# Kernel optimization log

Hardware: AMD Instinct MI355X
Metric: run time of the kernel (lower is better)

## Reference

```python
import jax, jax.numpy as jnp
import numpy as np

T, N, E, F_IN, H1, H2, NUM_GRAPHS, K = 8, 10000, 320000, 32, 32, 16, 64, 5


def setup_inputs() -> dict:
    key = jax.random.key(0)
    ks = jax.random.split(key, 16)
    p = lambda k, shape: jax.random.normal(k, shape, jnp.float32) * 0.05
    return {
        "x": jax.random.normal(ks[0], (T, N, F_IN), jnp.float32),
        "edge_index": jax.random.randint(ks[1], (2, E), 0, N),
        "edge_attr": jax.random.uniform(ks[2], (E,), jnp.float32),
        "batch": jnp.sort(jax.random.randint(ks[3], (N,), 0, NUM_GRAPHS)),
        "Wx1": p(ks[4], (4, K, F_IN, H1)),
        "bx1": jnp.zeros((4, H1), jnp.float32),
        "Wh1": p(ks[5], (4, K, H1, H1)),
        "bh1": jnp.zeros((4, H1), jnp.float32),
        "wc1": p(ks[6], (3, H1)),
        "b1": jnp.zeros((4, H1), jnp.float32),
        "Wx2": p(ks[7], (4, K, H1, H2)),
        "bx2": jnp.zeros((4, H2), jnp.float32),
        "Wh2": p(ks[8], (4, K, H2, H2)),
        "bh2": jnp.zeros((4, H2), jnp.float32),
        "wc2": p(ks[9], (3, H2)),
        "b2": jnp.zeros((4, H2), jnp.float32),
        "lin_w": p(ks[10], (H2, 1)),
        "lin_b": jnp.zeros((1,), jnp.float32),
    }


def _forward(x, edge_index, edge_attr, batch,
             Wx1, bx1, Wh1, bh1, wc1, b1,
             Wx2, bx2, Wh2, bh2, wc2, b2, lin_w, lin_b):
    src, dst = edge_index[0], edge_index[1]
    n = x.shape[1]

    # ChebConv sym normalization with lambda_max=2: L_hat = L_sym - I = -D^{-1/2} A D^{-1/2}
    deg = jax.ops.segment_sum(edge_attr, src, num_segments=n)
    deg_safe = jnp.where(deg > 0, deg, 1.0)
    dis = jnp.where(deg > 0, jax.lax.rsqrt(deg_safe), 0.0)
    wnorm = dis[src] * edge_attr * dis[dst]  # [E]

    def Lhat(z):  # z: [N, C] -> L_hat @ z
        return -jax.ops.segment_sum(wnorm[:, None] * z[src], dst, num_segments=n)

    def cheb(z, W, b):  # W: [K, C_in, C_out], b: [C_out]
        out = z @ W[0]
        Tp, Tc = z, Lhat(z)  # T_0, T_1
        out = out + Tc @ W[1]
        for k in range(2, W.shape[0]):
            Tp, Tc = Tc, 2.0 * Lhat(Tc) - Tp
            out = out + Tc @ W[k]
        return out + b

    def cell(X, H, C, Wx, bx, Wh, bh, wc, bg):
        # gate order: 0=i, 1=f, 2=c, 3=o (GConvLSTM with peepholes)
        I = jax.nn.sigmoid(cheb(X, Wx[0], bx[0]) + cheb(H, Wh[0], bh[0]) + wc[0] * C + bg[0])
        Fg = jax.nn.sigmoid(cheb(X, Wx[1], bx[1]) + cheb(H, Wh[1], bh[1]) + wc[1] * C + bg[1])
        Ct = jnp.tanh(cheb(X, Wx[2], bx[2]) + cheb(H, Wh[2], bh[2]) + bg[2])
        Cn = Fg * C + I * Ct
        O = jax.nn.sigmoid(cheb(X, Wx[3], bx[3]) + cheb(H, Wh[3], bh[3]) + wc[2] * Cn + bg[3])
        return O * jnp.tanh(Cn), Cn

    @jax.checkpoint
    def step(carry, xt):
        h1, c1, h2, c2 = carry
        h1, c1 = cell(xt, h1, c1, Wx1, bx1, Wh1, bh1, wc1, b1)
        h2, c2 = cell(h1, h2, c2, Wx2, bx2, Wh2, bh2, wc2, b2)
        return (h1, c1, h2, c2), None

    z32 = jnp.zeros((n, Wh1.shape[-1]), x.dtype)
    z16 = jnp.zeros((n, Wh2.shape[-1]), x.dtype)
    (h1, c1, h2, c2), _ = jax.lax.scan(step, (z32, z32, z16, z16), x)

    # relu/dropout on h2 in the torch code is dead code (its result is unused in eval)
    u = jax.ops.segment_sum(h2, batch, num_segments=NUM_GRAPHS)  # global_add_pool
    return (u @ lin_w + lin_b).reshape(-1)


def reference(x, edge_index, edge_attr, batch,
              Wx1, bx1, Wh1, bh1, wc1, b1,
              Wx2, bx2, Wh2, bh2, wc2, b2, lin_w, lin_b):
    return _forward(x, edge_index, edge_attr, batch,
                    Wx1, bx1, Wh1, bh1, wc1, b1,
                    Wx2, bx2, Wh2, bh2, wc2, b2, lin_w, lin_b)
```

## Files before the change

kernel.cpp:

```cpp
#include <hip/hip_runtime.h>
#include <hip/hip_bf16.h>

#define TT 8
#define NN 10000
#define EE 320000
#define NG 64
#define SZS 400
#define SZH 384

typedef short v8s __attribute__((ext_vector_type(8)));
typedef _Float16 v8h __attribute__((ext_vector_type(8)));
typedef float v4f __attribute__((ext_vector_type(4)));

__device__ __forceinline__ float sigmf(float x){ return 1.f/(1.f+expf(-x)); }
__device__ __forceinline__ unsigned short f2h(float f){ _Float16 h=(_Float16)f; return __builtin_bit_cast(unsigned short,h); }
__device__ __forceinline__ float h2f(unsigned short s){ return (float)__builtin_bit_cast(_Float16,s); }
__device__ __forceinline__ unsigned pack2h(float x,float y){ return (unsigned)f2h(x) | ((unsigned)f2h(y)<<16); }
__device__ __forceinline__ size_t fragidx(int TK,int row,int c){
  int tile=row>>4, m=row&15, kt=c>>5, cc=c&31;
  return ((size_t)(tile*TK+kt)*64 + (cc>>3)*16 + m)*8 + (cc&7);
}

__global__ void k_deg(const int* __restrict__ src, const float* __restrict__ ea, float* __restrict__ deg){
  int e = blockIdx.x*256 + threadIdx.x;
  if(e<EE) atomicAdd(&deg[src[e]], ea[e]);
}

__global__ void k_dis(const float* __restrict__ deg, float* __restrict__ dis){
  int n = blockIdx.x*256+threadIdx.x;
  if(n<NN){ float d=deg[n]; dis[n] = d>0.f ? rsqrtf(d) : 0.f; }
}

__global__ void k_wnorm(const int* __restrict__ src, const int* __restrict__ dst, const float* __restrict__ ea,
                        const float* __restrict__ dis, float* __restrict__ wnorm, int* __restrict__ cnt){
  int e = blockIdx.x*256+threadIdx.x;
  if(e<EE){
    int s=src[e], d=dst[e];
    wnorm[e] = dis[s]*ea[e]*dis[d];
    atomicAdd(&cnt[d],1);
  }
}

__global__ __launch_bounds__(1024) void k_scan(const int* __restrict__ cnt, int* __restrict__ rowptr, int* __restrict__ wp){
  __shared__ int wsum[16];
  __shared__ int carrysh;
  int tid=threadIdx.x, lane=tid&63, wv=tid>>6;
  if(tid==0){ carrysh=0; rowptr[0]=0; }
  __syncthreads();
  for(int base=0;base<NN;base+=1024){
    int i=base+tid;
    int v=(i<NN)?cnt[i]:0;
    int s=v;
    #pragma unroll
    for(int d=1;d<64;d<<=1){ int t=__shfl_up(s,d,64); if(lane>=d) s+=t; }
    if(lane==63) wsum[wv]=s;
    __syncthreads();
    if(wv==0 && lane<16){
      int t=wsum[lane]; int ss=t;
      #pragma unroll
      for(int d=1;d<16;d<<=1){ int u=__shfl_up(ss,d,64); if(lane>=d) ss+=u; }
      wsum[lane]=ss-t;
    }
    __syncthreads();
    int total = carrysh + wsum[wv] + s;
    if(i<NN) rowptr[i+1]=total;
    __syncthreads();
    if(tid==1023) carrysh = total;
    __syncthreads();
  }
  for(int i=tid;i<NN;i+=1024) wp[i]=rowptr[i];
}

__global__ void k_scatter(const int* __restrict__ src, const int* __restrict__ dst, const float* __restrict__ wnorm,
                          int* __restrict__ wp, int2* __restrict__ pack){
  int e = blockIdx.x*256+threadIdx.x;
  if(e<EE){
    int d=dst[e];
    int pos = atomicAdd(&wp[d],1);
    pack[pos] = make_int2(src[e], __float_as_int(wnorm[e]));
  }
}

__device__ __forceinline__ float fetchW1(const float* Wx, const float* Wh, int kk, int col){
  int g=col>>5, j=col&31;
  if(kk<160){ int k=kk>>5, i=kk&31; return Wx[((g*5+k)*32+i)*32+j]; }
  int rr=kk-160; int k=rr>>5, i=rr&31; return Wh[((g*5+k)*32+i)*32+j];
}
__device__ __forceinline__ float fetchW2(const float* Wx, const float* Wh, int kk, int col){
  int g=col>>4, j=col&15;
  if(kk<160){ int k=kk>>5, i=kk&31; return Wx[((g*5+k)*32+i)*16+j]; }
  if(kk<240){ int rr=kk-160; int k=rr>>4, i=rr&15; return Wh[((g*5+k)*16+i)*16+j]; }
  return 0.f;
}

__global__ void k_wreorg(const float* __restrict__ Wx1,const float* __restrict__ bx1,
                         const float* __restrict__ Wh1,const float* __restrict__ bh1,const float* __restrict__ b1,
                         const float* __restrict__ Wx2,const float* __restrict__ bx2,
                         const float* __restrict__ Wh2,const float* __restrict__ bh2,const float* __restrict__ b2g,
                         short* __restrict__ Wpk1, short* __restrict__ Wpk2,
                         float* __restrict__ Bc1,float* __restrict__ Bc2){
  int idx = blockIdx.x*256+threadIdx.x;
  if(idx < 5120){
    int lane=idx&63, rest=idx>>6;
    int nt=rest&7, kt=rest>>3;
    int col = nt*16 + (lane&15);
    int g = lane>>4;
    #pragma unroll
    for(int j=0;j<8;j++){
      int kk = kt*32 + 8*g + j;
      Wpk1[(size_t)idx*8+j]=(short)f2h(fetchW1(Wx1,Wh1,kk,col));
    }
  } else if(idx < 7168){
    int t=idx-5120;
    int lane=t&63, rest=t>>6;
    int nt=rest&3, kt=rest>>2;
    int col = nt*16 + (lane&15);
    int g = lane>>4;
    #pragma unroll
    for(int j=0;j<8;j++){
      int kk = kt*32 + 8*g + j;
      Wpk2[(size_t)t*8+j]=(short)f2h(fetchW2(Wx2,Wh2,kk,col));
    }
  } else if(idx < 7296){
    int i=idx-7168; int g=i>>5,j=i&31;
    Bc1[i]=bx1[g*32+j]+bh1[g*32+j]+b1[g*32+j];
  } else if(idx < 7360){
    int i=idx-7296; int g=i>>4,j=i&15;
    Bc2[i]=bx2[g*16+j]+bh2[g*16+j]+b2g[g*16+j];
  }
}

__global__ void k_init1(const float* __restrict__ xt, float* __restrict__ ZS,
                        unsigned short* __restrict__ ZH, short* __restrict__ Zb1){
  int idx=blockIdx.x*256+threadIdx.x;
  if(idx<NN*8){
    int n=idx>>3, c4=idx&7;
    float4 v = ((const float4*)xt)[idx];
    *(float4*)&ZS[(size_t)n*SZS + 240 + c4*4] = v;
    unsigned p0=pack2h(v.x,v.y), p1=pack2h(v.z,v.w);
    *(unsigned*)&ZH[(size_t)n*SZH + 48 + c4*4]     = p0;
    *(unsigned*)&ZH[(size_t)n*SZH + 48 + c4*4 + 2] = p1;
    size_t fi = fragidx(5, n, c4*4);
    *(unsigned*)&Zb1[fi]   = p0;
    *(unsigned*)&Zb1[fi+2] = p1;
  }
}

template<int MODE>
__global__ __launch_bounds__(256) void k_spmm(const int* __restrict__ rowptr, const int2* __restrict__ pack,
    float* __restrict__ ZS, unsigned short* __restrict__ ZH,
    short* __restrict__ Zb1, short* __restrict__ Zb2, int k){
  int wlocal = __builtin_amdgcn_readfirstlane(threadIdx.x>>6);
  int wid = blockIdx.x*4 + wlocal;
  if(wid>=NN) return;
  int l = threadIdx.x&63;
  int ch; bool act;
  if(MODE==0){ ch=48+2*l; act=(l<16); }
  else if(MODE==1){
    if(l<16) ch=2*l; else if(l<24) ch=32+2*(l-16); else ch=48+2*(l-24);
    act=(l<40);
  } else {
    if(l<16) ch=2*l; else ch=32+2*(l-16);
    act=(l<24);
  }
  if(!act) ch=(MODE==2)?0:48;
  int cin_h = (k-1)*96 + ch;
  int base,width,cloc;
  if(ch<32){ base=0; width=32; cloc=ch; }
  else if(ch<48){ base=160; width=16; cloc=ch-32; }
  else { base=240; width=32; cloc=ch-48; }
  int cout = base + k*width + cloc;
  int cpp  = base + (k-2)*width + cloc;
  const unsigned short* __restrict__ Zc = ZH + cin_h;
  int e0=rowptr[wid], e1=rowptr[wid+1];
  float accx=0.f, accy=0.f;
  int e=e0;
  for(; e+16<=e1; e+=16){
    float w[16]; unsigned z[16];
    #pragma unroll
    for(int j=0;j<16;j++){
      int2 p=pack[e+j];
      w[j]=__int_as_float(p.y);
      z[j]=*(const unsigned*)&Zc[(unsigned)p.x*SZH];
    }
    #pragma unroll
    for(int j=0;j<16;j++){
      accx += h2f((unsigned short)(z[j]&0xffffu))*w[j];
      accy += h2f((unsigned short)(z[j]>>16))*w[j];
    }
  }
  for(; e+4<=e1; e+=4){
    float w[4]; unsigned z[4];
    #pragma unroll
    for(int j=0;j<4;j++){ int2 p=pack[e+j]; w[j]=__int_as_float(p.y); z[j]=*(const unsigned*)&Zc[(unsigned)p.x*SZH]; }
    #pragma unroll
    for(int j=0;j<4;j++){
      accx += h2f((unsigned short)(z[j]&0xffffu))*w[j];
      accy += h2f((unsigned short)(z[j]>>16))*w[j];
    }
  }
  for(; e<e1; ++e){
    int2 p=pack[e];
    unsigned zz=*(const unsigned*)&Zc[(unsigned)p.x*SZH];
    float ww=__int_as_float(p.y);
    accx += h2f((unsigned short)(zz&0xffffu))*ww;
    accy += h2f((unsigned short)(zz>>16))*ww;
  }
  if(act){
    float alpha=(k==1)?1.f:2.f;
    float vx = -alpha*accx, vy = -alpha*accy;
    if(k>=2){
      float2 pp=*(const float2*)&ZS[(unsigned)wid*SZS+cpp];
      vx -= pp.x; vy -= pp.y;
    }
    *(float2*)&ZS[(unsigned)wid*SZS+cout]=make_float2(vx,vy);
    unsigned hh = pack2h(vx,vy);
    if(k<=3) *(unsigned*)&ZH[(size_t)wid*SZH + k*96 + ch] = hh;
    if(ch<48) *(unsigned*)&Zb2[fragidx(8,wid,cout)] = hh;
    else      *(unsigned*)&Zb1[fragidx(5,wid,cout-240)] = hh;
  }
}

__global__ __launch_bounds__(256) void k_gemm1(const short* Zb1r, const short* Zb2r, const short* __restrict__ Wpk,
        const float* __restrict__ Bc, const float* __restrict__ wc1,
        float* __restrict__ c1, float* __restrict__ ZS, unsigned short* __restrict__ ZH,
        short* Zb1w, short* Zb2w, const float* __restrict__ xn){
  int wv=threadIdx.x>>6, lane=threadIdx.x&63;
  int tile=blockIdx.x*4+wv;
  if(tile>=625) return;
  const v8s* A1=(const v8s*)Zb1r + (size_t)tile*320 + lane;
  const v8s* A2=(const v8s*)Zb2r + (size_t)tile*512 + lane;
  v8h afr[10];
  #pragma unroll
  for(int kt=0;kt<5;kt++){
    afr[kt]  =__builtin_bit_cast(v8h, A1[kt*64]);
    afr[5+kt]=__builtin_bit_cast(v8h, A2[kt*64]);
  }
  const v8s* Wp=(const v8s*)Wpk;
  v4f acc[8];
  #pragma unroll
  for(int nt=0;nt<8;nt++) acc[nt]=(v4f){0.f,0.f,0.f,0.f};
  #pragma unroll
  for(int kt=0;kt<10;kt++){
    #pragma unroll
    for(int nt=0;nt<8;nt++){
      v8h b=__builtin_bit_cast(v8h, Wp[(kt*8+nt)*64+lane]);
      acc[nt]=__builtin_amdgcn_mfma_f32_16x16x32_f16(afr[kt],b,acc[nt],0,0,0);
    }
  }
  int row0=tile*16;
  int j0=lane&15;
  int r0=row0+(lane>>4)*4;
  #pragma unroll
  for(int reg=0;reg<4;reg++){
    int row=r0+reg;
    #pragma unroll
    for(int jj=0;jj<2;jj++){
      int j=jj*16+j0;
      float c=c1[row*32+j];
      float I =sigmf(acc[0+jj][reg]+Bc[j]      + wc1[j]*c);
      float Fg=sigmf(acc[2+jj][reg]+Bc[32+j]   + wc1[32+j]*c);
      float Ct=tanhf(acc[4+jj][reg]+Bc[64+j]);
      float Cn=Fg*c + I*Ct;
      float O =sigmf(acc[6+jj][reg]+Bc[96+j]   + wc1[64+j]*Cn);
      float h =O*tanhf(Cn);
      c1[row*32+j]=Cn;
      ZS[(size_t)row*SZS + j]=h;
      ZH[(size_t)row*SZH + j]=f2h(h);
      Zb2w[fragidx(8,row,j)]=(short)f2h(h);
    }
    if(xn){
      float2 xv=*(const float2*)&xn[(size_t)row*32 + 2*j0];
      *(float2*)&ZS[(size_t)row*SZS + 240 + 2*j0]=xv;
      unsigned pr=pack2h(xv.x,xv.y);
      *(unsigned*)&ZH[(size_t)row*SZH + 48 + 2*j0]=pr;
      *(unsigned*)&Zb1w[fragidx(5,row,2*j0)]=pr;
    }
  }
}

__global__ __launch_bounds__(256) void k_gemm2(const short* Zb2r, const short* __restrict__ Wpk,
        const float* __restrict__ Bc, const float* __restrict__ wc2,
        float* __restrict__ c2, float* __restrict__ ZS, unsigned short* __restrict__ ZH,
        short* Zb2w, float* __restrict__ u, const int* __restrict__ batch, int last){
  int wv=threadIdx.x>>6, lane=threadIdx.x&63;
  int tile=blockIdx.x*4+wv;
  if(tile>=625) return;
  const v8s* Az=(const v8s*)Zb2r + (size_t)tile*512 + lane;
  v8h afr[8];
  #pragma unroll
  for(int kt=0;kt<8;kt++) afr[kt]=__builtin_bit_cast(v8h, Az[kt*64]);
  const v8s* Wp=(const v8s*)Wpk;
  v4f acc[4];
  #pragma unroll
  for(int nt=0;nt<4;nt++) acc[nt]=(v4f){0.f,0.f,0.f,0.f};
  #pragma unroll
  for(int kt=0;kt<8;kt++){
    #pragma unroll
    for(int nt=0;nt<4;nt++){
      v8h b=__builtin_bit_cast(v8h, Wp[(kt*4+nt)*64+lane]);
      acc[nt]=__builtin_amdgcn_mfma_f32_16x16x32_f16(afr[kt],b,acc[nt],0,0,0);
    }
  }
  int row0=tile*16;
  int j=lane&15;
  int r0=row0+(lane>>4)*4;
  #pragma unroll
  for(int reg=0;reg<4;reg++){
    int row=r0+reg;
    float c=c2[row*16+j];
    float I =sigmf(acc[0][reg]+Bc[j]    +wc2[j]*c);
    float Fg=sigmf(acc[1][reg]+Bc[16+j] +wc2[16+j]*c);
    float Ct=tanhf(acc[2][reg]+Bc[32+j]);
    float Cn=Fg*c+I*Ct;
    float O =sigmf(acc[3][reg]+Bc[48+j] +wc2[32+j]*Cn);
    float h =O*tanhf(Cn);
    c2[row*16+j]=Cn;
    ZS[(size_t)row*SZS + 160 + j]=h;
    ZH[(size_t)row*SZH + 32 + j]=f2h(h);
    Zb2w[fragidx(8,row,160+j)]=(short)f2h(h);
    if(last) atomicAdd(&u[batch[row]*16+j], h);
  }
}

__global__ void k_final(const float* __restrict__ u, const float* __restrict__ lw, const float* __restrict__ lb,
                        float* __restrict__ out){
  int g=threadIdx.x;
  if(g<NG){
    float s=lb[0];
    #pragma unroll
    for(int j=0;j<16;j++) s += u[g*16+j]*lw[j];
    out[g]=s;
  }
}

extern "C" void kernel_launch(void* const* d_in, const int* in_sizes, int n_in,
                              void* d_out, int out_size, void* d_ws, size_t ws_size,
                              hipStream_t stream){
  const float* x   = (const float*)d_in[0];
  const int*   ei  = (const int*)d_in[1];
  const float* ea  = (const float*)d_in[2];
  const int*   bat = (const int*)d_in[3];
  const float* Wx1=(const float*)d_in[4];  const float* bx1=(const float*)d_in[5];
  const float* Wh1=(const float*)d_in[6];  const float* bh1=(const float*)d_in[7];
  const float* wc1=(const float*)d_in[8];  const float* b1 =(const float*)d_in[9];
  const float* Wx2=(const float*)d_in[10]; const float* bx2=(const float*)d_in[11];
  const float* Wh2=(const float*)d_in[12]; const float* bh2=(const float*)d_in[13];
  const float* wc2=(const float*)d_in[14]; const float* b2 =(const float*)d_in[15];
  const float* lw =(const float*)d_in[16]; const float* lb =(const float*)d_in[17];
  const int* src = ei; const int* dst = ei+EE;

  float* ws = (float*)d_ws;
  size_t off=0;
  auto alloc=[&](size_t n)->float*{ float* p=ws+off; off+=(n+15)&~(size_t)15; return p; };
  float* deg=alloc(NN);
  float* c1=alloc((size_t)NN*32);
  float* c2=alloc((size_t)NN*16);
  float* u =alloc(NG*16);
  int*   cnt=(int*)alloc(NN);
  float* ZS=alloc((size_t)NN*SZS);
  unsigned short* ZH=(unsigned short*)alloc((size_t)NN*SZH/2);
  short* Zb1=(short*)alloc(625*5*64*8/2);
  short* Zb2=(short*)alloc(625*8*64*8/2);
  size_t zeroEnd=off;
  float* dis=alloc(NN);
  float* wnorm=alloc(EE);
  int*   rowptr=(int*)alloc(NN+1);
  int*   wp=(int*)alloc(NN);
  int2*  pack=(int2*)alloc((size_t)EE*2);
  short* Wpk1=(short*)alloc(5120*4);
  short* Wpk2=(short*)alloc(2048*4);
  float* Bc1=alloc(128);     float* Bc2=alloc(64);
  (void)ws_size; (void)in_sizes; (void)n_in; (void)out_size;

  hipMemsetAsync(d_ws, 0, zeroEnd*sizeof(float), stream);
  k_deg    <<<1250,256,0,stream>>>(src,ea,deg);
  k_dis    <<<40,256,0,stream>>>(deg,dis);
  k_wnorm  <<<1250,256,0,stream>>>(src,dst,ea,dis,wnorm,cnt);
  k_scan   <<<1,1024,0,stream>>>(cnt,rowptr,wp);
  k_scatter<<<1250,256,0,stream>>>(src,dst,wnorm,wp,pack);
  k_wreorg <<<29,256,0,stream>>>(Wx1,bx1,Wh1,bh1,b1,Wx2,bx2,Wh2,bh2,b2,Wpk1,Wpk2,Bc1,Bc2);

  k_init1<<<313,256,0,stream>>>(x, ZS, ZH, Zb1);
  for(int k=1;k<5;k++)
    k_spmm<0><<<2500,256,0,stream>>>(rowptr,pack,ZS,ZH,Zb1,Zb2,k);

  for(int t=0;t<TT;t++){
    k_gemm1<<<157,256,0,stream>>>(Zb1,Zb2,Wpk1,Bc1,wc1,c1,ZS,ZH,Zb1,Zb2,
          (t<TT-1)? x+(size_t)(t+1)*NN*32 : nullptr);
    if(t<TT-1){
      for(int k=1;k<5;k++)
        k_spmm<1><<<2500,256,0,stream>>>(rowptr,pack,ZS,ZH,Zb1,Zb2,k);
    } else {
      for(int k=1;k<5;k++)
        k_spmm<2><<<2500,256,0,stream>>>(rowptr,pack,ZS,ZH,Zb1,Zb2,k);
    }
    k_gemm2<<<157,256,0,stream>>>(Zb2,Wpk2,Bc2,wc2,c2,ZS,ZH,Zb2,u,bat,(t==TT-1)?1:0);
  }
  k_final<<<1,64,0,stream>>>(u,lw,lb,(float*)d_out);
}
```

Before: 661.5 us.

## Pack multiple nodes per wave in SpMM and fuse layer GEMMs across timesteps

```diff
diff --git a/kernel.cpp b/kernel.cpp
--- a/kernel.cpp
+++ b/kernel.cpp
@@ -150,92 +150,81 @@
 __global__ __launch_bounds__(256) void k_spmm(const int* __restrict__ rowptr, const int2* __restrict__ pack,
     float* __restrict__ ZS, unsigned short* __restrict__ ZH,
     short* __restrict__ Zb1, short* __restrict__ Zb2, int k){
-  int wlocal = __builtin_amdgcn_readfirstlane(threadIdx.x>>6);
-  int wid = blockIdx.x*4 + wlocal;
-  if(wid>=NN) return;
+  const int LPN = (MODE==0)?8 : (MODE==1)?20 : 12;
+  const int NPW = (MODE==0)?7 : (MODE==1)?3 : 5;
+  int wslot = (blockIdx.x*blockDim.x + threadIdx.x)>>6;
   int l = threadIdx.x&63;
-  int ch; bool act;
-  if(MODE==0){ ch=48+2*l; act=(l<16); }
-  else if(MODE==1){
-    if(l<16) ch=2*l; else if(l<24) ch=32+2*(l-16); else ch=48+2*(l-24);
-    act=(l<40);
-  } else {
-    if(l<16) ch=2*l; else ch=32+2*(l-16);
-    act=(l<24);
-  }
-  if(!act) ch=(MODE==2)?0:48;
-  int cin_h = (k-1)*96 + ch;
+  int sub = l/LPN;
+  int ln  = l - sub*LPN;
+  int wid = wslot*NPW + sub;
+  bool act = (sub<NPW) && (wid<NN);
+  int widc = act? wid : 0;
+  int ch = (MODE==0)? 48+ln*4 : ln*4;
   int base,width,cloc;
   if(ch<32){ base=0; width=32; cloc=ch; }
   else if(ch<48){ base=160; width=16; cloc=ch-32; }
   else { base=240; width=32; cloc=ch-48; }
-  int cout = base + k*width + cloc;
-  int cpp  = base + (k-2)*width + cloc;
-  const unsigned short* __restrict__ Zc = ZH + cin_h;
-  int e0=rowptr[wid], e1=rowptr[wid+1];
-  float accx=0.f, accy=0.f;
-  int e=e0;
-  for(; e+16<=e1; e+=16){
-    float w[16]; unsigned z[16];
-    #pragma unroll
-    for(int j=0;j<16;j++){
-      int2 p=pack[e+j];
-      w[j]=__int_as_float(p.y);
-      z[j]=*(const unsigned*)&Zc[(unsigned)p.x*SZH];
-    }
-    #pragma unroll
-    for(int j=0;j<16;j++){
-      accx += h2f((unsigned short)(z[j]&0xffffu))*w[j];
-      accy += h2f((unsigned short)(z[j]>>16))*w[j];
-    }
-  }
-  for(; e+4<=e1; e+=4){
-    float w[4]; unsigned z[4];
-    #pragma unroll
-    for(int j=0;j<4;j++){ int2 p=pack[e+j]; w[j]=__int_as_float(p.y); z[j]=*(const unsigned*)&Zc[(unsigned)p.x*SZH]; }
-    #pragma unroll
-    for(int j=0;j<4;j++){
-      accx += h2f((unsigned short)(z[j]&0xffffu))*w[j];
-      accy += h2f((unsigned short)(z[j]>>16))*w[j];
-    }
-  }
-  for(; e<e1; ++e){
-    int2 p=pack[e];
-    unsigned zz=*(const unsigned*)&Zc[(unsigned)p.x*SZH];
-    float ww=__int_as_float(p.y);
-    accx += h2f((unsigned short)(zz&0xffffu))*ww;
-    accy += h2f((unsigned short)(zz>>16))*ww;
+  int e0=rowptr[widc], e1=rowptr[widc+1];
+  int deg = act? (e1-e0) : 0;
+  int emax = e1-1; if(emax<e0) emax=e0; if(emax>EE-1) emax=EE-1;
+  const unsigned short* __restrict__ Zc = ZH + (size_t)(k-1)*96 + ch;
+  float a0=0.f,a1=0.f,a2=0.f,a3=0.f;
+  int b=0;
+  while(__any(b<deg)){
+    #pragma unroll
+    for(int j=0;j<8;j++){
+      int bj=b+j;
+      bool v = bj<deg;
+      int ee = v? (e0+bj) : emax;
+      int2 p = pack[ee];
+      float w = v? __int_as_float(p.y) : 0.f;
+      uint2 z = *(const uint2*)&Zc[(size_t)(unsigned)p.x*SZH];
+      a0 += h2f((unsigned short)(z.x&0xffffu))*w;
+      a1 += h2f((unsigned short)(z.x>>16))*w;
+      a2 += h2f((unsigned short)(z.y&0xffffu))*w;
+      a3 += h2f((unsigned short)(z.y>>16))*w;
+    }
+    b+=8;
   }
   if(act){
     float alpha=(k==1)?1.f:2.f;
-    float vx = -alpha*accx, vy = -alpha*accy;
+    float4 vv = make_float4(-alpha*a0,-alpha*a1,-alpha*a2,-alpha*a3);
+    int cout = base + k*width + cloc;
     if(k>=2){
-      float2 pp=*(const float2*)&ZS[(unsigned)wid*SZS+cpp];
-      vx -= pp.x; vy -= pp.y;
-    }
-    *(float2*)&ZS[(unsigned)wid*SZS+cout]=make_float2(vx,vy);
-    unsigned hh = pack2h(vx,vy);
-    if(k<=3) *(unsigned*)&ZH[(size_t)wid*SZH + k*96 + ch] = hh;
-    if(ch<48) *(unsigned*)&Zb2[fragidx(8,wid,cout)] = hh;
-    else      *(unsigned*)&Zb1[fragidx(5,wid,cout-240)] = hh;
-  }
-}
-
-__global__ __launch_bounds__(256) void k_gemm1(const short* Zb1r, const short* Zb2r, const short* __restrict__ Wpk,
-        const float* __restrict__ Bc, const float* __restrict__ wc1,
+      int cpp = base + (k-2)*width + cloc;
+      float4 pp=*(const float4*)&ZS[(size_t)wid*SZS+cpp];
+      vv.x-=pp.x; vv.y-=pp.y; vv.z-=pp.z; vv.w-=pp.w;
+    }
+    *(float4*)&ZS[(size_t)wid*SZS+cout]=vv;
+    unsigned h01=pack2h(vv.x,vv.y), h23=pack2h(vv.z,vv.w);
+    if(k<=3){
+      unsigned* zh=(unsigned*)&ZH[(size_t)wid*SZH + k*96 + ch];
+      zh[0]=h01; zh[1]=h23;
+    }
+    if(ch<48){
+      unsigned* zb=(unsigned*)&Zb2[fragidx(8,wid,cout)];
+      zb[0]=h01; zb[1]=h23;
+    } else {
+      unsigned* zb=(unsigned*)&Zb1[fragidx(5,wid,cout-240)];
+      zb[0]=h01; zb[1]=h23;
+    }
+  }
+}
+
+__device__ __forceinline__ void gemm1_dev(int tile,int lane,
+        const short* __restrict__ Zb1, const short* __restrict__ Zb2,
+        const v8s* __restrict__ H1T0r, v8s* __restrict__ H1T0w,
+        const short* __restrict__ Wpk, const float* __restrict__ Bc, const float* __restrict__ wc1,
         float* __restrict__ c1, float* __restrict__ ZS, unsigned short* __restrict__ ZH,
-        short* Zb1w, short* Zb2w, const float* __restrict__ xn){
-  int wv=threadIdx.x>>6, lane=threadIdx.x&63;
-  int tile=blockIdx.x*4+wv;
-  if(tile>=625) return;
-  const v8s* A1=(const v8s*)Zb1r + (size_t)tile*320 + lane;
-  const v8s* A2=(const v8s*)Zb2r + (size_t)tile*512 + lane;
+        short* __restrict__ Zb1w, const float* __restrict__ xn){
+  const v8s* A1=(const v8s*)Zb1 + (size_t)tile*320 + lane;
+  const v8s* A2=(const v8s*)Zb2 + (size_t)tile*512 + lane;
   v8h afr[10];
   #pragma unroll
-  for(int kt=0;kt<5;kt++){
-    afr[kt]  =__builtin_bit_cast(v8h, A1[kt*64]);
-    afr[5+kt]=__builtin_bit_cast(v8h, A2[kt*64]);
-  }
+  for(int kt=0;kt<5;kt++) afr[kt]=__builtin_bit_cast(v8h, A1[kt*64]);
+  afr[5]=__builtin_bit_cast(v8h, H1T0r[(size_t)tile*64+lane]);
+  #pragma unroll
+  for(int kt=1;kt<5;kt++) afr[5+kt]=__builtin_bit_cast(v8h, A2[kt*64]);
   const v8s* Wp=(const v8s*)Wpk;
   v4f acc[8];
   #pragma unroll
@@ -251,6 +240,7 @@
   int row0=tile*16;
   int j0=lane&15;
   int r0=row0+(lane>>4)*4;
+  unsigned short hfr[8];
   #pragma unroll
   for(int reg=0;reg<4;reg++){
     int row=r0+reg;
@@ -267,7 +257,7 @@
       c1[row*32+j]=Cn;
       ZS[(size_t)row*SZS + j]=h;
       ZH[(size_t)row*SZH + j]=f2h(h);
-      Zb2w[fragidx(8,row,j)]=(short)f2h(h);
+      ((unsigned short*)H1T0w)[fragidx(1,row,j)]=f2h(h);
     }
     if(xn){
       float2 xv=*(const float2*)&xn[(size_t)row*32 + 2*j0];
@@ -277,19 +267,19 @@
       *(unsigned*)&Zb1w[fragidx(5,row,2*j0)]=pr;
     }
   }
-}
-
-__global__ __launch_bounds__(256) void k_gemm2(const short* Zb2r, const short* __restrict__ Wpk,
-        const float* __restrict__ Bc, const float* __restrict__ wc2,
+  (void)hfr;
+}
+
+__device__ __forceinline__ void gemm2_dev(int tile,int lane,
+        const short* __restrict__ Zb2, const v8s* __restrict__ H1T0r,
+        const short* __restrict__ Wpk, const float* __restrict__ Bc, const float* __restrict__ wc2,
         float* __restrict__ c2, float* __restrict__ ZS, unsigned short* __restrict__ ZH,
-        short* Zb2w, float* __restrict__ u, const int* __restrict__ batch, int last){
-  int wv=threadIdx.x>>6, lane=threadIdx.x&63;
-  int tile=blockIdx.x*4+wv;
-  if(tile>=625) return;
-  const v8s* Az=(const v8s*)Zb2r + (size_t)tile*512 + lane;
+        short* __restrict__ Zb2w, float* __restrict__ u, const int* __restrict__ batch, int last){
+  const v8s* Az=(const v8s*)Zb2 + (size_t)tile*512 + lane;
   v8h afr[8];
-  #pragma unroll
-  for(int kt=0;kt<8;kt++) afr[kt]=__builtin_bit_cast(v8h, Az[kt*64]);
+  afr[0]=__builtin_bit_cast(v8h, H1T0r[(size_t)tile*64+lane]);
+  #pragma unroll
+  for(int kt=1;kt<8;kt++) afr[kt]=__builtin_bit_cast(v8h, Az[kt*64]);
   const v8s* Wp=(const v8s*)Wpk;
   v4f acc[4];
   #pragma unroll
@@ -320,6 +310,43 @@
     ZH[(size_t)row*SZH + 32 + j]=f2h(h);
     Zb2w[fragidx(8,row,160+j)]=(short)f2h(h);
     if(last) atomicAdd(&u[batch[row]*16+j], h);
+  }
+}
+
+__global__ __launch_bounds__(256) void k_g1(const short* Zb1, const short* Zb2,
+        const v8s* H1T0r, v8s* H1T0w, const short* Wpk1, const float* Bc1, const float* wc1,
+        float* c1, float* ZS, unsigned short* ZH, short* Zb1w, const float* xn){
+  int wv=threadIdx.x>>6, lane=threadIdx.x&63;
+  int tile=blockIdx.x*4+wv;
+  if(tile>=625) return;
+  gemm1_dev(tile,lane,Zb1,Zb2,H1T0r,H1T0w,Wpk1,Bc1,wc1,c1,ZS,ZH,Zb1w,xn);
+}
+
+__global__ __launch_bounds__(256) void k_g2(const short* Zb2, const v8s* H1T0r,
+        const short* Wpk2, const float* Bc2, const float* wc2,
+        float* c2, float* ZS, unsigned short* ZH, short* Zb2w,
+        float* u, const int* batch, int last){
+  int wv=threadIdx.x>>6, lane=threadIdx.x&63;
+  int tile=blockIdx.x*4+wv;
+  if(tile>=625) return;
+  gemm2_dev(tile,lane,Zb2,H1T0r,Wpk2,Bc2,wc2,c2,ZS,ZH,Zb2w,u,batch,last);
+}
+
+__global__ __launch_bounds__(256) void k_g12(const short* Zb1, const short* Zb2,
+        const v8s* H1T0r, v8s* H1T0w,
+        const short* Wpk1, const float* Bc1, const float* wc1, float* c1,
+        const short* Wpk2, const float* Bc2, const float* wc2, float* c2,
+        float* ZS, unsigned short* ZH, short* Zb1w, short* Zb2w,
+        const float* xn, float* u, const int* batch){
+  int wv=threadIdx.x>>6, lane=threadIdx.x&63;
+  if(blockIdx.x<157){
+    int tile=blockIdx.x*4+wv;
+    if(tile>=625) return;
+    gemm1_dev(tile,lane,Zb1,Zb2,H1T0r,H1T0w,Wpk1,Bc1,wc1,c1,ZS,ZH,Zb1w,xn);
+  } else {
+    int tile=(blockIdx.x-157)*4+wv;
+    if(tile>=625) return;
+    gemm2_dev(tile,lane,Zb2,H1T0r,Wpk2,Bc2,wc2,c2,ZS,ZH,Zb2w,u,batch,0);
   }
 }
 
@@ -362,6 +389,8 @@
   unsigned short* ZH=(unsigned short*)alloc((size_t)NN*SZH/2);
   short* Zb1=(short*)alloc(625*5*64*8/2);
   short* Zb2=(short*)alloc(625*8*64*8/2);
+  short* H1T0a=(short*)alloc(625*64*8/2);
+  short* H1T0b=(short*)alloc(625*64*8/2);
   size_t zeroEnd=off;
   float* dis=alloc(NN);
   float* wnorm=alloc(EE);
@@ -372,6 +401,7 @@
   short* Wpk2=(short*)alloc(2048*4);
   float* Bc1=alloc(128);     float* Bc2=alloc(64);
   (void)ws_size; (void)in_sizes; (void)n_in; (void)out_size;
+  v8s* H1T0[2] = { (v8s*)H1T0a, (v8s*)H1T0b };
 
   hipMemsetAsync(d_ws, 0, zeroEnd*sizeof(float), stream);
   k_deg    <<<1250,256,0,stream>>>(src,ea,deg);
@@ -383,19 +413,20 @@
 
   k_init1<<<313,256,0,stream>>>(x, ZS, ZH, Zb1);
   for(int k=1;k<5;k++)
-    k_spmm<0><<<2500,256,0,stream>>>(rowptr,pack,ZS,ZH,Zb1,Zb2,k);
-
-  for(int t=0;t<TT;t++){
-    k_gemm1<<<157,256,0,stream>>>(Zb1,Zb2,Wpk1,Bc1,wc1,c1,ZS,ZH,Zb1,Zb2,
-          (t<TT-1)? x+(size_t)(t+1)*NN*32 : nullptr);
-    if(t<TT-1){
-      for(int k=1;k<5;k++)
-        k_spmm<1><<<2500,256,0,stream>>>(rowptr,pack,ZS,ZH,Zb1,Zb2,k);
-    } else {
-      for(int k=1;k<5;k++)
-        k_spmm<2><<<2500,256,0,stream>>>(rowptr,pack,ZS,ZH,Zb1,Zb2,k);
-    }
-    k_gemm2<<<157,256,0,stream>>>(Zb2,Wpk2,Bc2,wc2,c2,ZS,ZH,Zb2,u,bat,(t==TT-1)?1:0);
-  }
+    k_spmm<0><<<358,256,0,stream>>>(rowptr,pack,ZS,ZH,Zb1,Zb2,k);
+
+  k_g1<<<157,256,0,stream>>>(Zb1,Zb2,H1T0[1],H1T0[0],Wpk1,Bc1,wc1,c1,ZS,ZH,Zb1, x+(size_t)NN*32);
+
+  for(int t=0;t<TT-1;t++){
+    for(int k=1;k<5;k++)
+      k_spmm<1><<<834,256,0,stream>>>(rowptr,pack,ZS,ZH,Zb1,Zb2,k);
+    k_g12<<<314,256,0,stream>>>(Zb1,Zb2,H1T0[t&1],H1T0[(t+1)&1],
+        Wpk1,Bc1,wc1,c1, Wpk2,Bc2,wc2,c2, ZS,ZH,Zb1,Zb2,
+        (t+2<TT)? x+(size_t)(t+2)*NN*32 : nullptr, u,bat);
+  }
+  for(int k=1;k<5;k++)
+    k_spmm<2><<<500,256,0,stream>>>(rowptr,pack,ZS,ZH,Zb1,Zb2,k);
+  k_g2<<<157,256,0,stream>>>(Zb2,H1T0[(TT-1)&1],Wpk2,Bc2,wc2,c2,ZS,ZH,Zb2,u,bat,1);
+
   k_final<<<1,64,0,stream>>>(u,lw,lb,(float*)d_out);
 }
```

After: 926.4 us. 40.0% more time.

## Fuse layer-2 gemm of step t with layer-1 gemm of step t+1 via double-buffered H1 tile

Applied to the files above, without the earlier changes.

```diff
diff --git a/kernel.cpp b/kernel.cpp
--- a/kernel.cpp
+++ b/kernel.cpp
@@ -221,21 +221,20 @@
   }
 }
 
-__global__ __launch_bounds__(256) void k_gemm1(const short* Zb1r, const short* Zb2r, const short* __restrict__ Wpk,
-        const float* __restrict__ Bc, const float* __restrict__ wc1,
+__device__ __forceinline__ void gemm1_dev(int tile,int lane,
+        const short* __restrict__ Zb1, const short* __restrict__ Zb2,
+        const v8s* __restrict__ H1T0r, v8s* __restrict__ H1T0w,
+        const short* __restrict__ Wpk, const float* __restrict__ Bc, const float* __restrict__ wc1,
         float* __restrict__ c1, float* __restrict__ ZS, unsigned short* __restrict__ ZH,
-        short* Zb1w, short* Zb2w, const float* __restrict__ xn){
-  int wv=threadIdx.x>>6, lane=threadIdx.x&63;
-  int tile=blockIdx.x*4+wv;
-  if(tile>=625) return;
-  const v8s* A1=(const v8s*)Zb1r + (size_t)tile*320 + lane;
-  const v8s* A2=(const v8s*)Zb2r + (size_t)tile*512 + lane;
+        short* __restrict__ Zb1w, const float* __restrict__ xn){
+  const v8s* A1=(const v8s*)Zb1 + (size_t)tile*320 + lane;
+  const v8s* A2=(const v8s*)Zb2 + (size_t)tile*512 + lane;
   v8h afr[10];
   #pragma unroll
-  for(int kt=0;kt<5;kt++){
-    afr[kt]  =__builtin_bit_cast(v8h, A1[kt*64]);
-    afr[5+kt]=__builtin_bit_cast(v8h, A2[kt*64]);
-  }
+  for(int kt=0;kt<5;kt++) afr[kt]=__builtin_bit_cast(v8h, A1[kt*64]);
+  afr[5]=__builtin_bit_cast(v8h, H1T0r[(size_t)tile*64+lane]);
+  #pragma unroll
+  for(int kt=1;kt<5;kt++) afr[5+kt]=__builtin_bit_cast(v8h, A2[kt*64]);
   const v8s* Wp=(const v8s*)Wpk;
   v4f acc[8];
   #pragma unroll
@@ -267,7 +266,7 @@
       c1[row*32+j]=Cn;
       ZS[(size_t)row*SZS + j]=h;
       ZH[(size_t)row*SZH + j]=f2h(h);
-      Zb2w[fragidx(8,row,j)]=(short)f2h(h);
+      ((unsigned short*)H1T0w)[fragidx(1,row,j)]=f2h(h);
     }
     if(xn){
       float2 xv=*(const float2*)&xn[(size_t)row*32 + 2*j0];
@@ -279,17 +278,16 @@
   }
 }
 
-__global__ __launch_bounds__(256) void k_gemm2(const short* Zb2r, const short* __restrict__ Wpk,
-        const float* __restrict__ Bc, const float* __restrict__ wc2,
+__device__ __forceinline__ void gemm2_dev(int tile,int lane,
+        const short* __restrict__ Zb2, const v8s* __restrict__ H1T0r,
+        const short* __restrict__ Wpk, const float* __restrict__ Bc, const float* __restrict__ wc2,
         float* __restrict__ c2, float* __restrict__ ZS, unsigned short* __restrict__ ZH,
-        short* Zb2w, float* __restrict__ u, const int* __restrict__ batch, int last){
-  int wv=threadIdx.x>>6, lane=threadIdx.x&63;
-  int tile=blockIdx.x*4+wv;
-  if(tile>=625) return;
-  const v8s* Az=(const v8s*)Zb2r + (size_t)tile*512 + lane;
+        short* __restrict__ Zb2w, float* __restrict__ u, const int* __restrict__ batch, int last){
+  const v8s* Az=(const v8s*)Zb2 + (size_t)tile*512 + lane;
   v8h afr[8];
-  #pragma unroll
-  for(int kt=0;kt<8;kt++) afr[kt]=__builtin_bit_cast(v8h, Az[kt*64]);
+  afr[0]=__builtin_bit_cast(v8h, H1T0r[(size_t)tile*64+lane]);
+  #pragma unroll
+  for(int kt=1;kt<8;kt++) afr[kt]=__builtin_bit_cast(v8h, Az[kt*64]);
   const v8s* Wp=(const v8s*)Wpk;
   v4f acc[4];
   #pragma unroll
@@ -320,6 +318,43 @@
     ZH[(size_t)row*SZH + 32 + j]=f2h(h);
     Zb2w[fragidx(8,row,160+j)]=(short)f2h(h);
     if(last) atomicAdd(&u[batch[row]*16+j], h);
+  }
+}
+
+__global__ __launch_bounds__(256) void k_g1(const short* Zb1, const short* Zb2,
+        const v8s* H1T0r, v8s* H1T0w, const short* Wpk1, const float* Bc1, const float* wc1,
+        float* c1, float* ZS, unsigned short* ZH, short* Zb1w, const float* xn){
+  int wv=threadIdx.x>>6, lane=threadIdx.x&63;
+  int tile=blockIdx.x*4+wv;
+  if(tile>=625) return;
+  gemm1_dev(tile,lane,Zb1,Zb2,H1T0r,H1T0w,Wpk1,Bc1,wc1,c1,ZS,ZH,Zb1w,xn);
+}
+
+__global__ __launch_bounds__(256) void k_g2(const short* Zb2, const v8s* H1T0r,
+        const short* Wpk2, const float* Bc2, const float* wc2,
+        float* c2, float* ZS, unsigned short* ZH, short* Zb2w,
+        float* u, const int* batch, int last){
+  int wv=threadIdx.x>>6, lane=threadIdx.x&63;
+  int tile=blockIdx.x*4+wv;
+  if(tile>=625) return;
+  gemm2_dev(tile,lane,Zb2,H1T0r,Wpk2,Bc2,wc2,c2,ZS,ZH,Zb2w,u,batch,last);
+}
+
+__global__ __launch_bounds__(256) void k_g12(const short* Zb1, const short* Zb2,
+        const v8s* H1T0r, v8s* H1T0w,
+        const short* Wpk1, const float* Bc1, const float* wc1, float* c1,
+        const short* Wpk2, const float* Bc2, const float* wc2, float* c2,
+        float* ZS, unsigned short* ZH, short* Zb1w, short* Zb2w,
+        const float* xn, float* u, const int* batch){
+  int wv=threadIdx.x>>6, lane=threadIdx.x&63;
+  if(blockIdx.x<157){
+    int tile=blockIdx.x*4+wv;
+    if(tile>=625) return;
+    gemm1_dev(tile,lane,Zb1,Zb2,H1T0r,H1T0w,Wpk1,Bc1,wc1,c1,ZS,ZH,Zb1w,xn);
+  } else {
+    int tile=(blockIdx.x-157)*4+wv;
+    if(tile>=625) return;
+    gemm2_dev(tile,lane,Zb2,H1T0r,Wpk2,Bc2,wc2,c2,ZS,ZH,Zb2w,u,batch,0);
   }
 }
 
@@ -362,6 +397,8 @@
   unsigned short* ZH=(unsigned short*)alloc((size_t)NN*SZH/2);
   short* Zb1=(short*)alloc(625*5*64*8/2);
   short* Zb2=(short*)alloc(625*8*64*8/2);
+  short* H1T0a=(short*)alloc(625*64*8/2);
+  short* H1T0b=(short*)alloc(625*64*8/2);
   size_t zeroEnd=off;
   float* dis=alloc(NN);
   float* wnorm=alloc(EE);
@@ -372,6 +409,7 @@
   short* Wpk2=(short*)alloc(2048*4);
   float* Bc1=alloc(128);     float* Bc2=alloc(64);
   (void)ws_size; (void)in_sizes; (void)n_in; (void)out_size;
+  v8s* H1T0[2] = { (v8s*)H1T0a, (v8s*)H1T0b };
 
   hipMemsetAsync(d_ws, 0, zeroEnd*sizeof(float), stream);
   k_deg    <<<1250,256,0,stream>>>(src,ea,deg);
@@ -385,17 +423,18 @@
   for(int k=1;k<5;k++)
     k_spmm<0><<<2500,256,0,stream>>>(rowptr,pack,ZS,ZH,Zb1,Zb2,k);
 
-  for(int t=0;t<TT;t++){
-    k_gemm1<<<157,256,0,stream>>>(Zb1,Zb2,Wpk1,Bc1,wc1,c1,ZS,ZH,Zb1,Zb2,
-          (t<TT-1)? x+(size_t)(t+1)*NN*32 : nullptr);
-    if(t<TT-1){
-      for(int k=1;k<5;k++)
-        k_spmm<1><<<2500,256,0,stream>>>(rowptr,pack,ZS,ZH,Zb1,Zb2,k);
-    } else {
-      for(int k=1;k<5;k++)
-        k_spmm<2><<<2500,256,0,stream>>>(rowptr,pack,ZS,ZH,Zb1,Zb2,k);
-    }
-    k_gemm2<<<157,256,0,stream>>>(Zb2,Wpk2,Bc2,wc2,c2,ZS,ZH,Zb2,u,bat,(t==TT-1)?1:0);
-  }
+  k_g1<<<157,256,0,stream>>>(Zb1,Zb2,H1T0[1],H1T0[0],Wpk1,Bc1,wc1,c1,ZS,ZH,Zb1, x+(size_t)NN*32);
+
+  for(int t=0;t<TT-1;t++){
+    for(int k=1;k<5;k++)
+      k_spmm<1><<<2500,256,0,stream>>>(rowptr,pack,ZS,ZH,Zb1,Zb2,k);
+    k_g12<<<314,256,0,stream>>>(Zb1,Zb2,H1T0[t&1],H1T0[(t+1)&1],
+        Wpk1,Bc1,wc1,c1, Wpk2,Bc2,wc2,c2, ZS,ZH,Zb1,Zb2,
+        (t+2<TT)? x+(size_t)(t+2)*NN*32 : nullptr, u,bat);
+  }
+  for(int k=1;k<5;k++)
+    k_spmm<2><<<2500,256,0,stream>>>(rowptr,pack,ZS,ZH,Zb1,Zb2,k);
+  k_g2<<<157,256,0,stream>>>(Zb2,H1T0[(TT-1)&1],Wpk2,Bc2,wc2,c2,ZS,ZH,Zb2,u,bat,1);
+
   k_final<<<1,64,0,stream>>>(u,lw,lb,(float*)d_out);
 }
```

Result: faster. 617.6 us (-6.6%).
